# Kernel optimization log

Measured on AMD Instinct MI355X. Metric: run time of the kernel, lower is better.

Reference implementation:

```python
import jax, jax.numpy as jnp
import numpy as np

B, N, D, H, F = 16, 257, 1024, 16, 4096
HD = D // H
EPS = 1e-5
GATING_TEMP = 0.25  # gating_hyperparam for steep_sigmoid
SCALE = HD ** -0.5


def layer_norm(x, g, b):
    mu = jnp.mean(x, axis=-1, keepdims=True)
    var = jnp.mean(jnp.square(x - mu), axis=-1, keepdims=True)
    return (x - mu) * jax.lax.rsqrt(var + EPS) * g + b


def quick_gelu(x):
    return x * jax.nn.sigmoid(1.702 * x)


def setup_inputs() -> dict:
    key = jax.random.key(0)
    ks = jax.random.split(key, 24)
    s = 0.02
    inp = {
        'hidden_states': jax.random.normal(ks[0], (B, N, D), jnp.float32),
        'cached_hidden': jax.random.normal(ks[1], (B, N, D), jnp.float32),
        'cached_q': jax.random.normal(ks[2], (B, N, D), jnp.float32),
        'cached_k': jax.random.normal(ks[3], (B, N, D), jnp.float32),
        'cached_v': jax.random.normal(ks[4], (B, N, D), jnp.float32),
        'ln1_g': jnp.ones((D,), jnp.float32),
        'ln1_b': jnp.zeros((D,), jnp.float32),
        'wq': jax.random.normal(ks[5], (D, D), jnp.float32) * s,
        'bq': jnp.zeros((D,), jnp.float32),
        'wk': jax.random.normal(ks[6], (D, D), jnp.float32) * s,
        'bk': jnp.zeros((D,), jnp.float32),
        'wv': jax.random.normal(ks[7], (D, D), jnp.float32) * s,
        'bv': jnp.zeros((D,), jnp.float32),
        'wo': jax.random.normal(ks[8], (D, D), jnp.float32) * s,
        'bo': jnp.zeros((D,), jnp.float32),
        'ln2_g': jnp.ones((D,), jnp.float32),
        'ln2_b': jnp.zeros((D,), jnp.float32),
        'w1': jax.random.normal(ks[9], (D, F), jnp.float32) * s,
        'b1': jnp.zeros((F,), jnp.float32),
        'w2': jax.random.normal(ks[10], (F, D), jnp.float32) * s,
        'b2': jnp.zeros((D,), jnp.float32),
        'threshold': jnp.float32(0.5),
    }
    return inp


def reference(hidden_states, cached_hidden, cached_q, cached_k, cached_v,
              ln1_g, ln1_b, wq, bq, wk, bk, wv, bv, wo, bo,
              ln2_g, ln2_b, w1, b1, w2, b2, threshold):
    # layer_norm1 + QKV projection (layer_norm1_qkv_projection)
    h_ln = layer_norm(hidden_states, ln1_g, ln1_b)
    q = h_ln @ wq + bq
    k = h_ln @ wk + bk
    v = h_ln @ wv + bv

    # reuse module: cosine^1 similarity vs cached hidden, steep_sigmoid gating
    # against learned threshold; soft gather/scatter blend of cached states.
    num = jnp.sum(cached_hidden * hidden_states, axis=-1)           # [B,N]
    den = (jnp.linalg.norm(cached_hidden, axis=-1)
           * jnp.linalg.norm(hidden_states, axis=-1) + 1e-8)
    sim = num / den                                                 # [B,N]
    gate = jax.nn.sigmoid((sim - threshold) / GATING_TEMP)[..., None]  # [B,N,1]

    hidden = gate * cached_hidden + (1.0 - gate) * hidden_states
    q = gate * cached_q + (1.0 - gate) * q
    k = gate * cached_k + (1.0 - gate) * k
    v = gate * cached_v + (1.0 - gate) * v

    # manual bmm-softmax-bmm attention
    qh = (q * SCALE).reshape(B, N, H, HD).transpose(0, 2, 1, 3)  # [B,H,N,hd]
    kh = k.reshape(B, N, H, HD).transpose(0, 2, 1, 3)
    vh = v.reshape(B, N, H, HD).transpose(0, 2, 1, 3)
    scores = jnp.einsum('bhqd,bhkd->bhqk', qh, kh)
    probs = jax.nn.softmax(scores, axis=-1)
    attn = jnp.einsum('bhqk,bhkd->bhqd', probs, vh)
    attn = attn.transpose(0, 2, 1, 3).reshape(B, N, D)
    attn = attn @ wo + bo

    hidden = hidden + attn
    residual = hidden
    hidden = layer_norm(hidden, ln2_g, ln2_b)
    hidden = quick_gelu(hidden @ w1 + b1) @ w2 + b2
    return residual + hidden
```

## Files before the change

kernel.cpp:

```cpp
#include <hip/hip_runtime.h>
#include <hip/hip_bf16.h>
#include <stdint.h>

#define BB   16
#define SEQ  257
#define DD   1024
#define NH   16
#define HD_  64
#define FF   4096
#define MM   (BB*SEQ)
#define MPAD 4224
#define SPAD 272
#define VPAD 288
#define SCALE_Q 0.125f

typedef __bf16 bf16x8 __attribute__((ext_vector_type(8)));
typedef float  f32x4  __attribute__((ext_vector_type(4)));
typedef unsigned short u16;

__device__ __forceinline__ u16 f2bf(float f) {
  uint32_t u = __float_as_uint(f);
  uint32_t r = (u + 0x7FFFu + ((u >> 16) & 1u)) >> 16;
  return (u16)r;
}
__device__ __forceinline__ void gll16(const void* g, void* l) {
  __builtin_amdgcn_global_load_lds(
      (const __attribute__((address_space(1))) void*)g,
      (__attribute__((address_space(3))) void*)l, 16, 0, 0);
}
__device__ __forceinline__ float wsum(float v) {
  #pragma unroll
  for (int o = 1; o < 64; o <<= 1) v += __shfl_xor(v, o);
  return v;
}

__global__ __launch_bounds__(256) void transpose_kernel(
    const float* __restrict__ in, u16* __restrict__ out, int R, int C) {
  __shared__ float tile[64][65];
  int ctiles = C >> 6;
  int r0 = (blockIdx.x / ctiles) << 6, c0 = (blockIdx.x % ctiles) << 6;
  int tx = threadIdx.x & 63, ty = threadIdx.x >> 6;
  #pragma unroll
  for (int it = 0; it < 16; ++it) {
    int rr = it * 4 + ty;
    tile[rr][tx] = in[(size_t)(r0 + rr) * C + c0 + tx];
  }
  __syncthreads();
  #pragma unroll
  for (int it = 0; it < 16; ++it) {
    int rr = it * 4 + ty;
    out[(size_t)(c0 + rr) * R + r0 + tx] = f2bf(tile[tx][rr]);
  }
}

__global__ __launch_bounds__(256) void vtrans_kernel(
    const u16* __restrict__ vb, u16* __restrict__ vt) {
  __shared__ u16 tile[64][72];
  const int bh = blockIdx.x, c = blockIdx.y;
  const int tx = threadIdx.x & 63, ty = threadIdx.x >> 6;
  const u16* src = vb + (size_t)bh * SPAD * HD_;
  u16* dst = vt + (size_t)bh * HD_ * VPAD;
  #pragma unroll
  for (int it = 0; it < 16; ++it) {
    int r = it * 4 + ty;
    int nn = c * 64 + r;  int nnc = nn < SPAD ? nn : SPAD - 1;
    tile[r][tx] = src[(size_t)nnc * HD_ + tx];
  }
  __syncthreads();
  #pragma unroll
  for (int it = 0; it < 16; ++it) {
    int hd = it * 4 + ty;
    int col = c * 64 + tx;
    if (col < VPAD) dst[(size_t)hd * VPAD + col] = tile[tx][hd];
  }
}

__global__ __launch_bounds__(256) void ln1_gate_kernel(
    const float* __restrict__ h, const float* __restrict__ c,
    const float* __restrict__ g, const float* __restrict__ bta,
    const float* __restrict__ thr, u16* __restrict__ hln,
    float* __restrict__ hblend, float* __restrict__ gate) {
  int m = blockIdx.x, t = threadIdx.x, l = t & 63, w = t >> 6;
  const float4 hv = *(const float4*)(h + (size_t)m * DD + t * 4);
  const float4 cv = *(const float4*)(c + (size_t)m * DD + t * 4);
  float sh = hv.x + hv.y + hv.z + hv.w;
  float sh2 = hv.x*hv.x + hv.y*hv.y + hv.z*hv.z + hv.w*hv.w;
  float sch = hv.x*cv.x + hv.y*cv.y + hv.z*cv.z + hv.w*cv.w;
  float sc2 = cv.x*cv.x + cv.y*cv.y + cv.z*cv.z + cv.w*cv.w;
  sh = wsum(sh); sh2 = wsum(sh2); sch = wsum(sch); sc2 = wsum(sc2);
  __shared__ float red[4][4];
  if (l == 0) { red[w][0]=sh; red[w][1]=sh2; red[w][2]=sch; red[w][3]=sc2; }
  __syncthreads();
  float Sh  = red[0][0]+red[1][0]+red[2][0]+red[3][0];
  float Sh2 = red[0][1]+red[1][1]+red[2][1]+red[3][1];
  float Sch = red[0][2]+red[1][2]+red[2][2]+red[3][2];
  float Sc2 = red[0][3]+red[1][3]+red[2][3]+red[3][3];
  float mean = Sh * (1.f/DD);
  float var  = Sh2 * (1.f/DD) - mean*mean;
  float rs   = rsqrtf(var + 1e-5f);
  float sim  = Sch / (sqrtf(Sc2)*sqrtf(Sh2) + 1e-8f);
  float gv   = 1.f / (1.f + __expf(-(sim - thr[0]) * 4.0f));
  float4 gg = *(const float4*)(g + t*4);
  float4 bb = *(const float4*)(bta + t*4);
  ushort4 ob;
  ob.x = f2bf((hv.x-mean)*rs*gg.x + bb.x);
  ob.y = f2bf((hv.y-mean)*rs*gg.y + bb.y);
  ob.z = f2bf((hv.z-mean)*rs*gg.z + bb.z);
  ob.w = f2bf((hv.w-mean)*rs*gg.w + bb.w);
  *(ushort4*)(hln + (size_t)m * DD + t * 4) = ob;
  float4 hb;
  hb.x = gv*cv.x + (1.f-gv)*hv.x;  hb.y = gv*cv.y + (1.f-gv)*hv.y;
  hb.z = gv*cv.z + (1.f-gv)*hv.z;  hb.w = gv*cv.w + (1.f-gv)*hv.w;
  *(float4*)(hblend + (size_t)m * DD + t * 4) = hb;
  if (t == 0) gate[m] = gv;
}

__global__ __launch_bounds__(256) void ln2_kernel(
    const float* __restrict__ in, const float* __restrict__ g,
    const float* __restrict__ bta, u16* __restrict__ outb) {
  int m = blockIdx.x, t = threadIdx.x, l = t & 63, w = t >> 6;
  const float4 hv = *(const float4*)(in + (size_t)m * DD + t * 4);
  float sh = hv.x + hv.y + hv.z + hv.w;
  float sh2 = hv.x*hv.x + hv.y*hv.y + hv.z*hv.z + hv.w*hv.w;
  sh = wsum(sh); sh2 = wsum(sh2);
  __shared__ float red[4][2];
  if (l == 0) { red[w][0] = sh; red[w][1] = sh2; }
  __syncthreads();
  float Sh  = red[0][0]+red[1][0]+red[2][0]+red[3][0];
  float Sh2 = red[0][1]+red[1][1]+red[2][1]+red[3][1];
  float mean = Sh * (1.f/DD);
  float rs = rsqrtf(Sh2 * (1.f/DD) - mean*mean + 1e-5f);
  float4 gg = *(const float4*)(g + t*4);
  float4 bb = *(const float4*)(bta + t*4);
  ushort4 ob;
  ob.x = f2bf((hv.x-mean)*rs*gg.x + bb.x);
  ob.y = f2bf((hv.y-mean)*rs*gg.y + bb.y);
  ob.z = f2bf((hv.z-mean)*rs*gg.z + bb.z);
  ob.w = f2bf((hv.w-mean)*rs*gg.w + bb.w);
  *(ushort4*)(outb + (size_t)m * DD + t * 4) = ob;
}

template<int EPI>
__global__ __launch_bounds__(256) void gemm_bt(
    const u16* __restrict__ A, const u16* __restrict__ Bt, int K,
    const float* __restrict__ bias,
    const float* __restrict__ gate,
    const float* __restrict__ c0, const float* __restrict__ c1, const float* __restrict__ c2,
    const float* __restrict__ bq, const float* __restrict__ bk, const float* __restrict__ bv,
    u16* __restrict__ qb, u16* __restrict__ kb, u16* __restrict__ vb,
    const float* __restrict__ addsrc, float* __restrict__ outf, u16* __restrict__ outb) {
  const int tid = threadIdx.x, w = tid >> 6, l = tid & 63, lr = l & 15, lh = l >> 4;
  const int n0 = blockIdx.x * 128, m0 = blockIdx.y * 128;
  const int wm = w >> 1, wn = w & 1;
  __shared__ u16 sA[2][4096], sB[2][4096];
  f32x4 acc[4][4];
  f32x4 zero = {0.f, 0.f, 0.f, 0.f};
  #pragma unroll
  for (int i = 0; i < 4; ++i)
    #pragma unroll
    for (int j = 0; j < 4; ++j) acc[i][j] = zero;

  const int r0 = tid >> 2, cc = (tid & 3) * 8;
  const u16* ga0 = A  + (size_t)(m0 + r0) * K + cc;
  const u16* ga1 = A  + (size_t)(m0 + 64 + r0) * K + cc;
  const u16* gb0 = Bt + (size_t)(n0 + r0) * K + cc;
  const u16* gb1 = Bt + (size_t)(n0 + 64 + r0) * K + cc;

  const int nt = K >> 5;
  gll16(ga0, &sA[0][w*512]);  gll16(ga1, &sA[0][2048 + w*512]);
  gll16(gb0, &sB[0][w*512]);  gll16(gb1, &sB[0][2048 + w*512]);

  for (int t = 0; t < nt; ++t) {
    const int cur = t & 1;
    __syncthreads();
    if (t + 1 < nt) {
      const int k0 = (t + 1) << 5;
      gll16(ga0 + k0, &sA[cur^1][w*512]);  gll16(ga1 + k0, &sA[cur^1][2048 + w*512]);
      gll16(gb0 + k0, &sB[cur^1][w*512]);  gll16(gb1 + k0, &sB[cur^1][2048 + w*512]);
    }
    bf16x8 af[4], bfr[4];
    #pragma unroll
    for (int mi = 0; mi < 4; ++mi)
      af[mi] = *(const bf16x8*)&sA[cur][(wm*64 + mi*16 + lr)*32 + lh*8];
    #pragma unroll
    for (int ni = 0; ni < 4; ++ni)
      bfr[ni] = *(const bf16x8*)&sB[cur][(wn*64 + ni*16 + lr)*32 + lh*8];
    #pragma unroll
    for (int mi = 0; mi < 4; ++mi)
      #pragma unroll
      for (int ni = 0; ni < 4; ++ni)
        acc[mi][ni] = __builtin_amdgcn_mfma_f32_16x16x32_bf16(af[mi], bfr[ni], acc[mi][ni], 0, 0, 0);
  }

  if constexpr (EPI == 0) {
    const int which = n0 >> 10;
    const float* cb = which==0 ? bq : (which==1 ? bk : bv);
    const float* cp = which==0 ? c0 : (which==1 ? c1 : c2);
    u16* dst = which==0 ? qb : (which==1 ? kb : vb);
    const float scl = which==0 ? SCALE_Q : 1.0f;
    #pragma unroll
    for (int mi = 0; mi < 4; ++mi) {
      #pragma unroll
      for (int r = 0; r < 4; ++r) {
        const int row = m0 + wm*64 + mi*16 + lh*4 + r;
        if (row < MM) {
          const float gv = gate[row];
          const int bidx = row / SEQ, nn = row - bidx * SEQ;
          #pragma unroll
          for (int ni = 0; ni < 4; ++ni) {
            const int col = n0 + wn*64 + ni*16 + lr;
            const int d = col & 1023, hd = d & 63, hh = d >> 6;
            const float lin = acc[mi][ni][r] + cb[d];
            const float val = (gv * cp[(size_t)row*DD + d] + (1.f - gv) * lin) * scl;
            dst[((size_t)(bidx*NH + hh)*SPAD + nn)*HD_ + hd] = f2bf(val);
          }
        }
      }
    }
  } else if constexpr (EPI == 1) {
    #pragma unroll
    for (int mi = 0; mi < 4; ++mi)
      #pragma unroll
      for (int r = 0; r < 4; ++r) {
        const int row = m0 + wm*64 + mi*16 + lh*4 + r;
        if (row < MM) {
          #pragma unroll
          for (int ni = 0; ni < 4; ++ni) {
            const int col = n0 + wn*64 + ni*16 + lr;
            outf[(size_t)row*DD + col] = acc[mi][ni][r] + bias[col] + addsrc[(size_t)row*DD + col];
          }
        }
      }
  } else {
    #pragma unroll
    for (int mi = 0; mi < 4; ++mi)
      #pragma unroll
      for (int r = 0; r < 4; ++r) {
        const int row = m0 + wm*64 + mi*16 + lh*4 + r;
        if (row < MM) {
          #pragma unroll
          for (int ni = 0; ni < 4; ++ni) {
            const int col = n0 + wn*64 + ni*16 + lr;
            const float x = acc[mi][ni][r] + bias[col];
            const float s = 1.f / (1.f + __expf(-1.702f * x));
            outb[(size_t)row*FF + col] = f2bf(x * s);
          }
        }
      }
  }
}

__global__ __launch_bounds__(256) void attn_kernel(
    const u16* __restrict__ qb, const u16* __restrict__ kb,
    const u16* __restrict__ vt, u16* __restrict__ attn_out) {
  __shared__ u16 P[64 * 296];
  const int bh = blockIdx.x, b = bh >> 4, hh = bh & 15;
  const int q0 = blockIdx.y * 64;
  const int tid = threadIdx.x, w = tid >> 6, l = tid & 63, lr = l & 15, lh = l >> 4;
  const u16* qp = qb + (size_t)bh * SPAD * HD_;
  const u16* kp = kb + (size_t)bh * SPAD * HD_;
  const u16* vp = vt + (size_t)bh * HD_ * VPAD;

  const int qr = q0 + w*16 + lr;
  const int qrc = qr < 271 ? qr : 271;
  bf16x8 aq0 = *(const bf16x8*)(qp + (size_t)qrc*HD_ + lh*8);
  bf16x8 aq1 = *(const bf16x8*)(qp + (size_t)qrc*HD_ + 32 + lh*8);

  f32x4 st[18];
  f32x4 zero = {0.f,0.f,0.f,0.f};
  #pragma unroll
  for (int t = 0; t < 18; ++t) st[t] = zero;
  #pragma unroll
  for (int t = 0; t < 18; ++t) {
    int key = t*16 + lr;  int keyc = key < 271 ? key : 271;
    bf16x8 b0 = *(const bf16x8*)(kp + (size_t)keyc*HD_ + lh*8);
    bf16x8 b1 = *(const bf16x8*)(kp + (size_t)keyc*HD_ + 32 + lh*8);
    st[t] = __builtin_amdgcn_mfma_f32_16x16x32_bf16(aq0, b0, st[t], 0, 0, 0);
    st[t] = __builtin_amdgcn_mfma_f32_16x16x32_bf16(aq1, b1, st[t], 0, 0, 0);
  }
  #pragma unroll
  for (int t = 0; t < 18; ++t) {
    int key = t*16 + lr;
    if (key >= SEQ) { st[t][0]=-1e30f; st[t][1]=-1e30f; st[t][2]=-1e30f; st[t][3]=-1e30f; }
  }
  float mr[4], sr[4];
  #pragma unroll
  for (int r = 0; r < 4; ++r) {
    float m = st[0][r];
    #pragma unroll
    for (int t = 1; t < 18; ++t) m = fmaxf(m, st[t][r]);
    m = fmaxf(m, __shfl_xor(m, 1));  m = fmaxf(m, __shfl_xor(m, 2));
    m = fmaxf(m, __shfl_xor(m, 4));  m = fmaxf(m, __shfl_xor(m, 8));
    mr[r] = m;  sr[r] = 0.f;
  }
  #pragma unroll
  for (int t = 0; t < 18; ++t)
    #pragma unroll
    for (int r = 0; r < 4; ++r) {
      float p = __expf(st[t][r] - mr[r]);
      st[t][r] = p;  sr[r] += p;
    }
  #pragma unroll
  for (int r = 0; r < 4; ++r) {
    sr[r] += __shfl_xor(sr[r], 1);  sr[r] += __shfl_xor(sr[r], 2);
    sr[r] += __shfl_xor(sr[r], 4);  sr[r] += __shfl_xor(sr[r], 8);
  }
  #pragma unroll
  for (int t = 0; t < 18; ++t)
    #pragma unroll
    for (int r = 0; r < 4; ++r)
      P[(w*16 + lh*4 + r)*296 + t*16 + lr] = f2bf(st[t][r]);
  __syncthreads();

  f32x4 o[4];
  #pragma unroll
  for (int ni = 0; ni < 4; ++ni) o[ni] = zero;
  #pragma unroll
  for (int ks = 0; ks < 9; ++ks) {
    bf16x8 pa = *(const bf16x8*)&P[(w*16 + lr)*296 + ks*32 + lh*8];
    #pragma unroll
    for (int ni = 0; ni < 4; ++ni) {
      bf16x8 bv_ = *(const bf16x8*)(vp + (size_t)(ni*16 + lr)*VPAD + ks*32 + lh*8);
      o[ni] = __builtin_amdgcn_mfma_f32_16x16x32_bf16(pa, bv_, o[ni], 0, 0, 0);
    }
  }
  #pragma unroll
  for (int r = 0; r < 4; ++r) {
    const int qrow = q0 + w*16 + lh*4 + r;
    if (qrow < SEQ) {
      const float inv = 1.f / sr[r];
      #pragma unroll
      for (int ni = 0; ni < 4; ++ni)
        attn_out[(size_t)(b*SEQ + qrow)*DD + hh*HD_ + ni*16 + lr] = f2bf(o[ni][r] * inv);
    }
  }
}

extern "C" void kernel_launch(void* const* d_in, const int* in_sizes, int n_in,
                              void* d_out, int out_size, void* d_ws, size_t ws_size,
                              hipStream_t stream) {
  (void)in_sizes; (void)n_in; (void)out_size; (void)ws_size;
  const float* hidden   = (const float*)d_in[0];
  const float* cached_h = (const float*)d_in[1];
  const float* cached_q = (const float*)d_in[2];
  const float* cached_k = (const float*)d_in[3];
  const float* cached_v = (const float*)d_in[4];
  const float* ln1_g = (const float*)d_in[5];
  const float* ln1_b = (const float*)d_in[6];
  const float* wq = (const float*)d_in[7];
  const float* bq = (const float*)d_in[8];
  const float* wk = (const float*)d_in[9];
  const float* bk = (const float*)d_in[10];
  const float* wv = (const float*)d_in[11];
  const float* bv = (const float*)d_in[12];
  const float* wo = (const float*)d_in[13];
  const float* bo = (const float*)d_in[14];
  const float* ln2_g = (const float*)d_in[15];
  const float* ln2_b = (const float*)d_in[16];
  const float* w1 = (const float*)d_in[17];
  const float* b1 = (const float*)d_in[18];
  const float* w2 = (const float*)d_in[19];
  const float* b2 = (const float*)d_in[20];
  const float* thr = (const float*)d_in[21];
  float* out = (float*)d_out;

  char* ws = (char*)d_ws;
  size_t off = 0;
  auto alloc = [&](size_t bytes) {
    void* p = ws + off;  off += (bytes + 255) & ~(size_t)255;  return p;
  };
  u16*   wqkvT  = (u16*)alloc(3072ull * 1024 * 2);
  u16*   woT    = (u16*)alloc(1024ull * 1024 * 2);
  u16*   w1T    = (u16*)alloc(4096ull * 1024 * 2);
  u16*   w2T    = (u16*)alloc(1024ull * 4096 * 2);
  float* gate   = (float*)alloc((size_t)MPAD * 4);
  float* resid2 = (float*)alloc((size_t)MPAD * DD * 4);
  u16*   regA   = (u16*)alloc((size_t)MPAD * DD * 2);
  u16 *hln = regA, *attn_o = regA, *ln2out = regA;
  const size_t QKV_B = (size_t)256 * SPAD * HD_ * 2;
  const size_t VT_B  = (size_t)256 * HD_ * VPAD * 2;
  char*  regB   = (char*)alloc(3*QKV_B + VT_B + (size_t)MPAD * DD * 4);
  u16*   qbuf   = (u16*)regB;
  u16*   kbuf   = (u16*)(regB + QKV_B);
  u16*   vbuf   = (u16*)(regB + 2*QKV_B);
  u16*   vtb    = (u16*)(regB + 3*QKV_B);
  float* hblend = (float*)(regB + 3*QKV_B + VT_B);
  u16*   mid    = (u16*)regB;

  dim3 blk(256);
  transpose_kernel<<<dim3(256),  blk, 0, stream>>>(wq, wqkvT,                 1024, 1024);
  transpose_kernel<<<dim3(256),  blk, 0, stream>>>(wk, wqkvT + 1024*1024,     1024, 1024);
  transpose_kernel<<<dim3(256),  blk, 0, stream>>>(wv, wqkvT + 2*1024*1024,   1024, 1024);
  transpose_kernel<<<dim3(256),  blk, 0, stream>>>(wo, woT,                   1024, 1024);
  transpose_kernel<<<dim3(1024), blk, 0, stream>>>(w1, w1T,                   1024, 4096);
  transpose_kernel<<<dim3(1024), blk, 0, stream>>>(w2, w2T,                   4096, 1024);

  ln1_gate_kernel<<<dim3(MM), blk, 0, stream>>>(hidden, cached_h, ln1_g, ln1_b, thr,
                                                hln, hblend, gate);

  gemm_bt<0><<<dim3(24, 33), blk, 0, stream>>>(hln, wqkvT, 1024, nullptr,
      gate, cached_q, cached_k, cached_v, bq, bk, bv, qbuf, kbuf, vbuf,
      nullptr, nullptr, nullptr);

  vtrans_kernel<<<dim3(256, 5), blk, 0, stream>>>(vbuf, vtb);

  attn_kernel<<<dim3(256, 5), blk, 0, stream>>>(qbuf, kbuf, vtb, attn_o);

  gemm_bt<1><<<dim3(8, 33), blk, 0, stream>>>(attn_o, woT, 1024, bo,
      nullptr, nullptr, nullptr, nullptr, nullptr, nullptr, nullptr,
      nullptr, nullptr, nullptr, hblend, resid2, nullptr);

  ln2_kernel<<<dim3(MM), blk, 0, stream>>>(resid2, ln2_g, ln2_b, ln2out);

  gemm_bt<2><<<dim3(32, 33), blk, 0, stream>>>(ln2out, w1T, 1024, b1,
      nullptr, nullptr, nullptr, nullptr, nullptr, nullptr, nullptr,
      nullptr, nullptr, nullptr, nullptr, nullptr, mid);

  gemm_bt<1><<<dim3(8, 33), blk, 0, stream>>>(mid, w2T, 4096, b2,
      nullptr, nullptr, nullptr, nullptr, nullptr, nullptr, nullptr,
      nullptr, nullptr, nullptr, resid2, out, nullptr);
}
```

Before: 332.7 us.

## Use 256x256 pipelined GEMM for QKV and MLP, split-K for down-proj

Adds a 512-thread GEMM kernel with 256x256 tiles, 64-wide K steps and an 8-phase interleave of async global-to-LDS loads, MFMA and barriers with priority hints. It is used for the QKV projection, the MLP up-projection and the MLP down-projection. The down-projection is split four ways along K, writing bf16 partials that a new reduce kernel sums with the bias and residual. Larger tiles and the phased pipeline aim to cut load traffic per FLOP and hide memory latency. The cost is bf16 rounding of the partial sums, extra partial-buffer traffic and padding rows out to 4352.

```diff
diff --git a/kernel.cpp b/kernel.cpp
--- a/kernel.cpp
+++ b/kernel.cpp
@@ -9,7 +9,7 @@
 #define HD_  64
 #define FF   4096
 #define MM   (BB*SEQ)
-#define MPAD 4224
+#define MPAD2 4352
 #define SPAD 272
 #define VPAD 288
 #define SCALE_Q 0.125f
@@ -22,6 +22,9 @@
   uint32_t u = __float_as_uint(f);
   uint32_t r = (u + 0x7FFFu + ((u >> 16) & 1u)) >> 16;
   return (u16)r;
+}
+__device__ __forceinline__ float bf2f(u16 u) {
+  return __uint_as_float(((uint32_t)u) << 16);
 }
 __device__ __forceinline__ void gll16(const void* g, void* l) {
   __builtin_amdgcn_global_load_lds(
@@ -140,15 +143,186 @@
   *(ushort4*)(outb + (size_t)m * DD + t * 4) = ob;
 }
 
+#define VMW4 do { asm volatile("s_waitcnt vmcnt(4)" ::: "memory"); \
+                  __builtin_amdgcn_sched_barrier(0); } while(0)
+#define VMW0 do { asm volatile("s_waitcnt vmcnt(0)" ::: "memory"); \
+                  __builtin_amdgcn_sched_barrier(0); } while(0)
+
+#define STG_A(T_, KS_, SLOT_) do { \
+  const u16* _g = pA + (T_)*64 + (KS_)*32; \
+  gll16(_g, &sA[SLOT_][KS_][0] + tid*8); \
+  gll16(_g + rowStep, &sA[SLOT_][KS_][0] + 4096 + tid*8); } while(0)
+#define STG_B(T_, KS_, SLOT_) do { \
+  const u16* _g = pB + (T_)*64 + (KS_)*32; \
+  gll16(_g, &sB[SLOT_][KS_][0] + tid*8); \
+  gll16(_g + rowStep, &sB[SLOT_][KS_][0] + 4096 + tid*8); } while(0)
+
+#define PHASE(SLOT_, KS_, MH_, RB_, STG_STMT, VM_STMT) do { \
+  { const u16* _pa = &sA[SLOT_][KS_][aBase + (MH_)*2048]; \
+    av[0] = *(const bf16x8*)(_pa);      av[1] = *(const bf16x8*)(_pa+512); \
+    av[2] = *(const bf16x8*)(_pa+1024); av[3] = *(const bf16x8*)(_pa+1536); } \
+  if (RB_) { const u16* _pb = &sB[SLOT_][KS_][bBase]; \
+    fv[0] = *(const bf16x8*)(_pb);      fv[1] = *(const bf16x8*)(_pb+512); \
+    fv[2] = *(const bf16x8*)(_pb+1024); fv[3] = *(const bf16x8*)(_pb+1536); } \
+  STG_STMT; \
+  __builtin_amdgcn_s_barrier(); \
+  asm volatile("s_waitcnt lgkmcnt(0)" ::: "memory"); \
+  __builtin_amdgcn_sched_barrier(0); \
+  __builtin_amdgcn_s_setprio(1); \
+  _Pragma("unroll") \
+  for (int f = 0; f < 4; ++f) \
+    _Pragma("unroll") \
+    for (int n = 0; n < 4; ++n) \
+      acc[(MH_)*4+f][n] = __builtin_amdgcn_mfma_f32_16x16x32_bf16( \
+          av[f], fv[n], acc[(MH_)*4+f][n], 0, 0, 0); \
+  __builtin_amdgcn_s_setprio(0); \
+  VM_STMT; \
+  __builtin_amdgcn_s_barrier(); } while(0)
+
+template<int EPI, int KT>
+__global__ __launch_bounds__(512, 2) void gemm256(
+    const u16* __restrict__ A, const u16* __restrict__ Bt,
+    int Kstride, int kBase0,
+    const float* __restrict__ bias,
+    const float* __restrict__ gate,
+    const float* __restrict__ c0, const float* __restrict__ c1, const float* __restrict__ c2,
+    const float* __restrict__ bq, const float* __restrict__ bk, const float* __restrict__ bvp,
+    u16* __restrict__ qb, u16* __restrict__ kb, u16* __restrict__ vb,
+    u16* __restrict__ outb, u16* __restrict__ partb) {
+  const int tid = threadIdx.x, w = tid >> 6, l = tid & 63, lr = l & 15, lh = l >> 4;
+  const int wm = w >> 2, wn = w & 3;
+  const int n0 = blockIdx.x * 256, m0 = blockIdx.y * 256;
+  const int kBase = kBase0 + blockIdx.z * (KT * 64);
+
+  __shared__ u16 sA[2][2][8192];
+  __shared__ u16 sB[2][2][8192];
+
+  f32x4 acc[8][4];
+  f32x4 zero = {0.f, 0.f, 0.f, 0.f};
+  #pragma unroll
+  for (int i = 0; i < 8; ++i)
+    #pragma unroll
+    for (int j = 0; j < 4; ++j) acc[i][j] = zero;
+
+  const int rS = tid >> 2, cS = (tid & 3) * 8;
+  const u16* pA = A  + (size_t)(m0 + rS) * Kstride + kBase + cS;
+  const u16* pB = Bt + (size_t)(n0 + rS) * Kstride + kBase + cS;
+  const size_t rowStep = (size_t)128 * Kstride;
+
+  const int aBase = (wm*128 + lr) * 32 + lh * 8;
+  const int bBase = (wn*64  + lr) * 32 + lh * 8;
+  bf16x8 av[4], fv[4];
+
+  STG_A(0,0,0);  STG_B(0,0,0);
+  STG_A(0,1,0);  STG_B(0,1,0);
+  STG_A(1,0,1);  STG_B(1,0,1);
+  asm volatile("s_waitcnt vmcnt(4)" ::: "memory");
+  __builtin_amdgcn_sched_barrier(0);
+  __builtin_amdgcn_s_barrier();
+
+  #pragma unroll 1
+  for (int i = 0; i < KT/2 - 1; ++i) {
+    const int jB = 2*i+1, nA = 2*i+2, nB = 2*i+3;
+    PHASE(0,0,0,1, STG_A(jB,1,1), ((void)0));
+    PHASE(0,0,1,0, STG_B(jB,1,1), ((void)0));
+    PHASE(0,1,0,1, STG_A(nA,0,0), ((void)0));
+    PHASE(0,1,1,0, STG_B(nA,0,0), VMW4);
+    PHASE(1,0,0,1, STG_A(nA,1,0), ((void)0));
+    PHASE(1,0,1,0, STG_B(nA,1,0), ((void)0));
+    PHASE(1,1,0,1, STG_A(nB,0,1), ((void)0));
+    PHASE(1,1,1,0, STG_B(nB,0,1), VMW4);
+  }
+  PHASE(0,0,0,1, STG_A(KT-1,1,1), ((void)0));
+  PHASE(0,0,1,0, STG_B(KT-1,1,1), ((void)0));
+  PHASE(0,1,0,1, ((void)0), ((void)0));
+  PHASE(0,1,1,0, ((void)0), VMW0);
+  PHASE(1,0,0,1, ((void)0), ((void)0));
+  PHASE(1,0,1,0, ((void)0), ((void)0));
+  PHASE(1,1,0,1, ((void)0), ((void)0));
+  PHASE(1,1,1,0, ((void)0), ((void)0));
+
+  const int crow = m0 + wm*128, ccol = n0 + wn*64;
+  if constexpr (EPI == 0) {
+    const int which = n0 >> 10;
+    const float* cb = which==0 ? bq : (which==1 ? bk : bvp);
+    const float* cp = which==0 ? c0 : (which==1 ? c1 : c2);
+    u16* dst = which==0 ? qb : (which==1 ? kb : vb);
+    const float scl = which==0 ? SCALE_Q : 1.0f;
+    #pragma unroll
+    for (int mi = 0; mi < 8; ++mi)
+      #pragma unroll
+      for (int rr = 0; rr < 4; ++rr) {
+        const int row = crow + mi*16 + lh*4 + rr;
+        if (row < MM) {
+          const float gv = gate[row];
+          const int bidx = row / SEQ, nn = row - bidx * SEQ;
+          #pragma unroll
+          for (int ni = 0; ni < 4; ++ni) {
+            const int col = ccol + ni*16 + lr;
+            const int d = col & 1023, hd = d & 63, hh = d >> 6;
+            const float lin = acc[mi][ni][rr] + cb[d];
+            const float val = (gv * cp[(size_t)row*DD + d] + (1.f - gv) * lin) * scl;
+            dst[((size_t)(bidx*NH + hh)*SPAD + nn)*HD_ + hd] = f2bf(val);
+          }
+        }
+      }
+  } else if constexpr (EPI == 2) {
+    #pragma unroll
+    for (int mi = 0; mi < 8; ++mi)
+      #pragma unroll
+      for (int rr = 0; rr < 4; ++rr) {
+        const int row = crow + mi*16 + lh*4 + rr;
+        if (row < MM) {
+          #pragma unroll
+          for (int ni = 0; ni < 4; ++ni) {
+            const int col = ccol + ni*16 + lr;
+            const float x = acc[mi][ni][rr] + bias[col];
+            const float s = 1.f / (1.f + __expf(-1.702f * x));
+            outb[(size_t)row*FF + col] = f2bf(x * s);
+          }
+        }
+      }
+  } else {
+    u16* pp = partb + (size_t)blockIdx.z * ((size_t)MPAD2 * 1024);
+    #pragma unroll
+    for (int mi = 0; mi < 8; ++mi)
+      #pragma unroll
+      for (int rr = 0; rr < 4; ++rr) {
+        const int row = crow + mi*16 + lh*4 + rr;
+        if (row < MM) {
+          #pragma unroll
+          for (int ni = 0; ni < 4; ++ni) {
+            const int col = ccol + ni*16 + lr;
+            pp[(size_t)row*1024 + col] = f2bf(acc[mi][ni][rr]);
+          }
+        }
+      }
+  }
+}
+
+__global__ __launch_bounds__(256) void reduce_mlp2(
+    const u16* __restrict__ parts, const float* __restrict__ bias,
+    const float* __restrict__ resid, float* __restrict__ out) {
+  const size_t PS = (size_t)MPAD2 * 1024;
+  const int row = blockIdx.x, t = threadIdx.x, c = t * 4;
+  const size_t base = (size_t)row * 1024 + c;
+  float4 r = *(const float4*)(resid + base);
+  float4 b = *(const float4*)(bias + c);
+  float o0 = r.x + b.x, o1 = r.y + b.y, o2 = r.z + b.z, o3 = r.w + b.w;
+  #pragma unroll
+  for (int p = 0; p < 4; ++p) {
+    ushort4 u = *(const ushort4*)(parts + p*PS + base);
+    o0 += bf2f(u.x);  o1 += bf2f(u.y);  o2 += bf2f(u.z);  o3 += bf2f(u.w);
+  }
+  float4 o;  o.x = o0;  o.y = o1;  o.z = o2;  o.w = o3;
+  *(float4*)(out + base) = o;
+}
+
 template<int EPI>
 __global__ __launch_bounds__(256) void gemm_bt(
     const u16* __restrict__ A, const u16* __restrict__ Bt, int K,
     const float* __restrict__ bias,
-    const float* __restrict__ gate,
-    const float* __restrict__ c0, const float* __restrict__ c1, const float* __restrict__ c2,
-    const float* __restrict__ bq, const float* __restrict__ bk, const float* __restrict__ bv,
-    u16* __restrict__ qb, u16* __restrict__ kb, u16* __restrict__ vb,
-    const float* __restrict__ addsrc, float* __restrict__ outf, u16* __restrict__ outb) {
+    const float* __restrict__ addsrc, float* __restrict__ outf) {
   const int tid = threadIdx.x, w = tid >> 6, l = tid & 63, lr = l & 15, lh = l >> 4;
   const int n0 = blockIdx.x * 128, m0 = blockIdx.y * 128;
   const int wm = w >> 1, wn = w & 1;
@@ -192,62 +366,19 @@
         acc[mi][ni] = __builtin_amdgcn_mfma_f32_16x16x32_bf16(af[mi], bfr[ni], acc[mi][ni], 0, 0, 0);
   }
 
-  if constexpr (EPI == 0) {
-    const int which = n0 >> 10;
-    const float* cb = which==0 ? bq : (which==1 ? bk : bv);
-    const float* cp = which==0 ? c0 : (which==1 ? c1 : c2);
-    u16* dst = which==0 ? qb : (which==1 ? kb : vb);
-    const float scl = which==0 ? SCALE_Q : 1.0f;
-    #pragma unroll
-    for (int mi = 0; mi < 4; ++mi) {
-      #pragma unroll
-      for (int r = 0; r < 4; ++r) {
-        const int row = m0 + wm*64 + mi*16 + lh*4 + r;
-        if (row < MM) {
-          const float gv = gate[row];
-          const int bidx = row / SEQ, nn = row - bidx * SEQ;
-          #pragma unroll
-          for (int ni = 0; ni < 4; ++ni) {
-            const int col = n0 + wn*64 + ni*16 + lr;
-            const int d = col & 1023, hd = d & 63, hh = d >> 6;
-            const float lin = acc[mi][ni][r] + cb[d];
-            const float val = (gv * cp[(size_t)row*DD + d] + (1.f - gv) * lin) * scl;
-            dst[((size_t)(bidx*NH + hh)*SPAD + nn)*HD_ + hd] = f2bf(val);
-          }
+  #pragma unroll
+  for (int mi = 0; mi < 4; ++mi)
+    #pragma unroll
+    for (int r = 0; r < 4; ++r) {
+      const int row = m0 + wm*64 + mi*16 + lh*4 + r;
+      if (row < MM) {
+        #pragma unroll
+        for (int ni = 0; ni < 4; ++ni) {
+          const int col = n0 + wn*64 + ni*16 + lr;
+          outf[(size_t)row*DD + col] = acc[mi][ni][r] + bias[col] + addsrc[(size_t)row*DD + col];
         }
       }
     }
-  } else if constexpr (EPI == 1) {
-    #pragma unroll
-    for (int mi = 0; mi < 4; ++mi)
-      #pragma unroll
-      for (int r = 0; r < 4; ++r) {
-        const int row = m0 + wm*64 + mi*16 + lh*4 + r;
-        if (row < MM) {
-          #pragma unroll
-          for (int ni = 0; ni < 4; ++ni) {
-            const int col = n0 + wn*64 + ni*16 + lr;
-            outf[(size_t)row*DD + col] = acc[mi][ni][r] + bias[col] + addsrc[(size_t)row*DD + col];
-          }
-        }
-      }
-  } else {
-    #pragma unroll
-    for (int mi = 0; mi < 4; ++mi)
-      #pragma unroll
-      for (int r = 0; r < 4; ++r) {
-        const int row = m0 + wm*64 + mi*16 + lh*4 + r;
-        if (row < MM) {
-          #pragma unroll
-          for (int ni = 0; ni < 4; ++ni) {
-            const int col = n0 + wn*64 + ni*16 + lr;
-            const float x = acc[mi][ni][r] + bias[col];
-            const float s = 1.f / (1.f + __expf(-1.702f * x));
-            outb[(size_t)row*FF + col] = f2bf(x * s);
-          }
-        }
-      }
-  }
 }
 
 __global__ __launch_bounds__(256) void attn_kernel(
@@ -373,21 +504,24 @@
   u16*   woT    = (u16*)alloc(1024ull * 1024 * 2);
   u16*   w1T    = (u16*)alloc(4096ull * 1024 * 2);
   u16*   w2T    = (u16*)alloc(1024ull * 4096 * 2);
-  float* gate   = (float*)alloc((size_t)MPAD * 4);
-  float* resid2 = (float*)alloc((size_t)MPAD * DD * 4);
-  u16*   regA   = (u16*)alloc((size_t)MPAD * DD * 2);
+  float* gate   = (float*)alloc((size_t)MPAD2 * 4);
+  float* resid2 = (float*)alloc((size_t)MPAD2 * DD * 4);
+  u16*   regA   = (u16*)alloc((size_t)MPAD2 * DD * 2);
   u16 *hln = regA, *attn_o = regA, *ln2out = regA;
-  const size_t QKV_B = (size_t)256 * SPAD * HD_ * 2;
-  const size_t VT_B  = (size_t)256 * HD_ * VPAD * 2;
-  char*  regB   = (char*)alloc(3*QKV_B + VT_B + (size_t)MPAD * DD * 4);
+  const size_t QKV_B  = (size_t)256 * SPAD * HD_ * 2;
+  const size_t VT_B   = (size_t)256 * HD_ * VPAD * 2;
+  const size_t PART_B = (size_t)MPAD2 * 1024 * 2;
+  const size_t partsOff = 3*QKV_B + VT_B;
+  char*  regB   = (char*)alloc(partsOff + 4*PART_B);
   u16*   qbuf   = (u16*)regB;
   u16*   kbuf   = (u16*)(regB + QKV_B);
   u16*   vbuf   = (u16*)(regB + 2*QKV_B);
   u16*   vtb    = (u16*)(regB + 3*QKV_B);
-  float* hblend = (float*)(regB + 3*QKV_B + VT_B);
+  float* hblend = (float*)(regB + partsOff);
   u16*   mid    = (u16*)regB;
-
-  dim3 blk(256);
+  u16*   parts  = (u16*)(regB + partsOff);
+
+  dim3 blk(256), blk5(512);
   transpose_kernel<<<dim3(256),  blk, 0, stream>>>(wq, wqkvT,                 1024, 1024);
   transpose_kernel<<<dim3(256),  blk, 0, stream>>>(wk, wqkvT + 1024*1024,     1024, 1024);
   transpose_kernel<<<dim3(256),  blk, 0, stream>>>(wv, wqkvT + 2*1024*1024,   1024, 1024);
@@ -398,25 +532,24 @@
   ln1_gate_kernel<<<dim3(MM), blk, 0, stream>>>(hidden, cached_h, ln1_g, ln1_b, thr,
                                                 hln, hblend, gate);
 
-  gemm_bt<0><<<dim3(24, 33), blk, 0, stream>>>(hln, wqkvT, 1024, nullptr,
-      gate, cached_q, cached_k, cached_v, bq, bk, bv, qbuf, kbuf, vbuf,
-      nullptr, nullptr, nullptr);
+  gemm256<0,16><<<dim3(12, 17), blk5, 0, stream>>>(hln, wqkvT, 1024, 0,
+      nullptr, gate, cached_q, cached_k, cached_v, bq, bk, bv,
+      qbuf, kbuf, vbuf, nullptr, nullptr);
 
   vtrans_kernel<<<dim3(256, 5), blk, 0, stream>>>(vbuf, vtb);
-
   attn_kernel<<<dim3(256, 5), blk, 0, stream>>>(qbuf, kbuf, vtb, attn_o);
 
-  gemm_bt<1><<<dim3(8, 33), blk, 0, stream>>>(attn_o, woT, 1024, bo,
-      nullptr, nullptr, nullptr, nullptr, nullptr, nullptr, nullptr,
-      nullptr, nullptr, nullptr, hblend, resid2, nullptr);
+  gemm_bt<1><<<dim3(8, 33), blk, 0, stream>>>(attn_o, woT, 1024, bo, hblend, resid2);
 
   ln2_kernel<<<dim3(MM), blk, 0, stream>>>(resid2, ln2_g, ln2_b, ln2out);
 
-  gemm_bt<2><<<dim3(32, 33), blk, 0, stream>>>(ln2out, w1T, 1024, b1,
-      nullptr, nullptr, nullptr, nullptr, nullptr, nullptr, nullptr,
-      nullptr, nullptr, nullptr, nullptr, nullptr, mid);
-
-  gemm_bt<1><<<dim3(8, 33), blk, 0, stream>>>(mid, w2T, 4096, b2,
-      nullptr, nullptr, nullptr, nullptr, nullptr, nullptr, nullptr,
-      nullptr, nullptr, nullptr, resid2, out, nullptr);
-}
+  gemm256<2,16><<<dim3(16, 17), blk5, 0, stream>>>(ln2out, w1T, 1024, 0,
+      b1, nullptr, nullptr, nullptr, nullptr, nullptr, nullptr, nullptr,
+      nullptr, nullptr, nullptr, mid, nullptr);
+
+  gemm256<3,16><<<dim3(4, 17, 4), blk5, 0, stream>>>(mid, w2T, 4096, 0,
+      nullptr, nullptr, nullptr, nullptr, nullptr, nullptr, nullptr, nullptr,
+      nullptr, nullptr, nullptr, nullptr, parts);
+
+  reduce_mlp2<<<dim3(MM), blk, 0, stream>>>(parts, b2, resid2, out);
+}
```

Result: slower. 363.6 us (+9.3%).
